# Optimization experiments

Hardware: AMD Instinct MI355X
Metric: run time of the kernel (lower is better)

Reference implementation:

```python
import jax, jax.numpy as jnp
import numpy as np

R = 50000          # residues
P = 24             # residue_pad_length
APR = 15           # atoms per residue (<= P)
N = R * APR        # total atoms
ACD = ATD = RCD = RID = 32
N_ATOM_CODES, N_ATOM_TYPES, N_RES_CODES, MAX_SEQ = 38, 6, 21, 1024
VEC_OUT, SC_OUT = 64, 256          # irreps_out = 64x1e + 256x0e
SC_IN = P * ACD + P * ATD + RCD + RID  # 1600 scalar inputs


def setup_inputs() -> dict:
    key = jax.random.key(0)
    ks = jax.random.split(key, 10)
    return {
        "residue_base_coords": jax.random.normal(ks[0], (R, 3), jnp.float32),
        "residue_relative_coords": jax.random.normal(ks[1], (N, 3), jnp.float32),
        "residue_code_index": jax.random.randint(ks[2], (R,), 0, N_RES_CODES),
        "residue_sequence_index": jnp.arange(R) % MAX_SEQ,
        "atom_code_index": jax.random.randint(ks[3], (N,), 0, N_ATOM_CODES),
        "atom_type_index": jax.random.randint(ks[4], (N,), 0, N_ATOM_TYPES),
        "residue_index_atomwise": jnp.repeat(jnp.arange(R), APR),  # sorted, APR atoms each
        "W_atom_code": jax.random.normal(ks[5], (N_ATOM_CODES, ACD), jnp.float32),
        "W_atom_type": jax.random.normal(ks[6], (N_ATOM_TYPES, ATD), jnp.float32),
        "W_res_code": jax.random.normal(ks[7], (N_RES_CODES, RCD), jnp.float32),
        "W_res_idx": jax.random.normal(ks[8], (MAX_SEQ, RID), jnp.float32),
        "W_vec": jax.random.normal(jax.random.fold_in(key, 1), (P, VEC_OUT), jnp.float32),
        "W_sc": jax.random.normal(ks[9], (SC_IN, SC_OUT), jnp.float32),
    }


def reference(residue_base_coords, residue_relative_coords, residue_code_index,
              residue_sequence_index, atom_code_index, atom_type_index,
              residue_index_atomwise, W_atom_code, W_atom_type, W_res_code,
              W_res_idx, W_vec, W_sc):
    R_ = residue_base_coords.shape[0]
    P_ = W_vec.shape[0]
    N_ = residue_index_atomwise.shape[0]
    ri = residue_index_atomwise
    # vectorized replacement of the per-residue python loop:
    # position of each atom within its residue (residue_index_atomwise is sorted)
    offsets = jnp.searchsorted(ri, jnp.arange(R_))            # first atom of each residue
    pos = jnp.arange(N_) - offsets[ri]                        # [N]
    # scatter atoms into padded [R, P, ...] layout (pad slots stay 0, like F.pad)
    mask = jnp.zeros((R_, P_), bool).at[ri, pos].set(True)
    rel = jnp.zeros((R_, P_, 3), residue_relative_coords.dtype).at[ri, pos].set(residue_relative_coords)
    codes = jnp.zeros((R_, P_), atom_code_index.dtype).at[ri, pos].set(atom_code_index)
    types = jnp.zeros((R_, P_), atom_type_index.dtype).at[ri, pos].set(atom_type_index)
    maskf = mask.astype(W_atom_code.dtype)[..., None]
    # embedding lookups, masked (pad embeddings zeroed as in the torch code)
    ac = (W_atom_code[codes] * maskf).reshape(R_, -1)         # [R, P*ACD]
    at = (W_atom_type[types] * maskf).reshape(R_, -1)         # [R, P*ATD]
    rc = W_res_code[residue_code_index]                       # [R, RCD]
    rix = W_res_idx[residue_sequence_index]                   # [R, RID]
    scalars = jnp.concatenate([ac, at, rc, rix], axis=-1)     # [R, SC_IN]
    # e3nn o3.Linear: l=1 channels mix only with l=1 (Px1e -> VEC_OUTx1e),
    # l=0 channels mix only with l=0; path-normalized by sqrt(fan_in), no bias.
    out_vec = jnp.einsum('rpc,pm->rmc', rel, W_vec) / jnp.sqrt(jnp.float32(P_))
    out_sc = (scalars @ W_sc) / jnp.sqrt(jnp.float32(scalars.shape[-1]))
    features = jnp.concatenate([out_vec.reshape(R_, -1), out_sc], axis=-1)  # [R, 3*VEC_OUT+SC_OUT]
    return residue_base_coords, features  # ResidueState(coords, features)
```

## Files before the change

kernel.cpp:

```cpp
#include <hip/hip_runtime.h>
#include <stdint.h>

static constexpr int P       = 24;
static constexpr int EMB_D   = 32;
static constexpr int N_AC    = 38;
static constexpr int N_AT    = 6;
static constexpr int N_RC    = 21;
static constexpr int MAXSEQ  = 1024;
static constexpr int VEC_OUT = 64;
static constexpr int SC_OUT  = 256;
static constexpr int FEAT    = 3 * VEC_OUT + SC_OUT;
static constexpr int CT      = N_AC * N_AT;
static constexpr int NROWS   = P * CT;
static constexpr int ROWB    = SC_OUT * 2;
static constexpr uint32_t ZROWB = (uint32_t)NROWS * ROWB;
static constexpr uint32_t EOFS  = (uint32_t)N_RC * 512;

__device__ __forceinline__ unsigned short f2bf(float f) {
    uint32_t x = __float_as_uint(f);
    uint32_t r = (x + 0x7FFFu + ((x >> 16) & 1u)) >> 16;
    return (unsigned short)r;
}

__global__ __launch_bounds__(256) void k1_init_build(
        const float* __restrict__ Wac, const float* __restrict__ Wat,
        const float* __restrict__ Wrc, const float* __restrict__ Wri,
        const float* __restrict__ Wsc,
        float* __restrict__ Ec, float* __restrict__ Et,
        unsigned short* __restrict__ ErcH, unsigned short* __restrict__ ErixH,
        int* __restrict__ starts, int* __restrict__ ends, int R) {
    int b = blockIdx.x;
    const int initB = (R + 255) / 256;
    if (b < initB) {
        int i = b * 256 + threadIdx.x;
        if (i < R) { starts[i] = 0; ends[i] = 0; }
        return;
    }
    b -= initB;
    const float* Wemb; int n_emb, sc_base, idx, sect;
    if (b < P * N_AC) {
        Wemb = Wac; n_emb = N_AC; sc_base = 0; idx = b; sect = 0;
    } else if (b < P * N_AC + P * N_AT) {
        Wemb = Wat; n_emb = N_AT; sc_base = P * EMB_D; idx = b - P * N_AC; sect = 1;
    } else if (b < P * N_AC + P * N_AT + N_RC) {
        Wemb = Wrc; n_emb = N_RC; sc_base = 2 * P * EMB_D;
        idx = b - (P * N_AC + P * N_AT); sect = 2;
    } else {
        Wemb = Wri; n_emb = MAXSEQ; sc_base = 2 * P * EMB_D + EMB_D;
        idx = b - (P * N_AC + P * N_AT + N_RC); sect = 3;
    }
    int p = idx / n_emb, e = idx % n_emb;
    int o = threadIdx.x;
    const float* wrow = Wemb + (size_t)e * EMB_D;
    const float* scol = Wsc + (size_t)(sc_base + p * EMB_D) * SC_OUT + o;
    float s = 0.f;
#pragma unroll
    for (int d = 0; d < EMB_D; ++d) s += wrow[d] * scol[(size_t)d * SC_OUT];
    s *= 0.025f;
    if (sect == 0)      Ec[(size_t)idx * SC_OUT + o] = s;
    else if (sect == 1) Et[(size_t)idx * SC_OUT + o] = s;
    else if (sect == 2) ErcH[(size_t)idx * SC_OUT + o] = f2bf(s);
    else                ErixH[(size_t)idx * SC_OUT + o] = f2bf(s);
}

__global__ void k2_find_bounds(const int* __restrict__ ri, int* __restrict__ starts,
                               int* __restrict__ ends, int N) {
    int i = blockIdx.x * blockDim.x + threadIdx.x;
    if (i >= N) return;
    int r = ri[i];
    if (i == 0 || ri[i - 1] != r) starts[r] = i;
    if (i == N - 1 || ri[i + 1] != r) ends[r] = i + 1;
}

__global__ __launch_bounds__(256) void k3_fuse_prep(
        const float* __restrict__ Ec, const float* __restrict__ Et,
        unsigned short* __restrict__ Etab,
        const int* __restrict__ starts, const int* __restrict__ ends,
        const int* __restrict__ rcode, const int* __restrict__ rseq,
        const int* __restrict__ acode, const int* __restrict__ atype,
        const float* __restrict__ rel, const float* __restrict__ base,
        float* __restrict__ out_coords,
        int4* __restrict__ hdr, uint32_t* __restrict__ recArr, int R) {
    int b = blockIdx.x;
    if (b < NROWS + 1) {
        int o = threadIdx.x;
        if (b == NROWS) { Etab[(size_t)b * SC_OUT + o] = 0; return; }
        int j = b / CT, ct = b % CT, c = ct / N_AT, t = ct % N_AT;
        float s = Ec[((size_t)j * N_AC + c) * SC_OUT + o] +
                  Et[((size_t)j * N_AT + t) * SC_OUT + o];
        Etab[(size_t)b * SC_OUT + o] = f2bf(s);
        return;
    }
    b -= NROWS + 1;
    const int hdrB = (R + 255) >> 8;
    if (b < hdrB) {
        int i = b * 256 + threadIdx.x;
        if (i < R) {
            int st = starts[i];
            int c = ends[i] - st; if (c > P) c = P;
            hdr[i] = make_int4(st, c, rcode[i], rseq[i]);
        }
        return;
    }
    b -= hdrB;
    const int coordB = (3 * R + 1023) >> 10;
    if (b < coordB) {
        int i = b * 256 + threadIdx.x;
        int n4 = (3 * R) >> 2;
        if (i < n4)
            reinterpret_cast<float4*>(out_coords)[i] =
                reinterpret_cast<const float4*>(base)[i];
        if (i == n4) {
            for (int t = 4 * n4; t < 3 * R; ++t) out_coords[t] = base[t];
        }
        return;
    }
    b -= coordB;
    int i = b * 256 + threadIdx.x;
    if (i >= R * 64) return;
    int r = i >> 6, l = i & 63;
    int st = starts[r];
    int c = ends[r] - st; if (c > P) c = P;
    uint32_t out;
    if (l < 16) {
        out = ZROWB;
        if (l < c)
            out = (uint32_t)((l * CT + acode[st + l] * N_AT + atype[st + l]) * ROWB);
    } else {
        int idx = l - 16, k = idx / 3, cc = idx - k * 3;
        float v = 0.f;
        if (k < c) v = rel[(size_t)(st + k) * 3 + cc];
        out = __float_as_uint(v);
    }
    recArr[(size_t)r * 64 + l] = out;
}

struct F3 { float x, y, z; };

#define RELV(RV, I) (((I) & 3) == 0 ? RV[(I) >> 2].x : \
                     ((I) & 3) == 1 ? RV[(I) >> 2].y : \
                     ((I) & 3) == 2 ? RV[(I) >> 2].z : RV[(I) >> 2].w)

__global__ __launch_bounds__(256, 4) void k4_residue(
        const int4* __restrict__ hdr, const uint32_t* __restrict__ recArr,
        const unsigned char* __restrict__ tab,
        const unsigned char* __restrict__ ErcBase,
        const float* __restrict__ Wvec,
        const int* __restrict__ acode, const int* __restrict__ atype,
        const float* __restrict__ rel,
        float* __restrict__ out_feat, int R) {

    __shared__ float lds_w[16 * VEC_OUT];
    for (int t = threadIdx.x; t < 16 * VEC_OUT; t += 256) lds_w[t] = Wvec[t];
    __syncthreads();

    const int wave   = (blockIdx.x << 2) + (threadIdx.x >> 6);
    const int lane   = threadIdx.x & 63;
    const int b31    = lane & 31;
    const bool hiH   = lane >= 32;
    const uint32_t lo16 = (uint32_t)(b31 * 16);
    const int totalw = gridDim.x << 2;
    if (wave >= R) return;

    int j  = wave;
    int rr = __builtin_amdgcn_readfirstlane(j < R ? j : R - 1);
    uint32_t rec = recArr[(size_t)rr * 64 + (lane & 15)];
    int4 h = hdr[rr];

    while (true) {
        const float4* srel = reinterpret_cast<const float4*>(
            recArr + (size_t)rr * 64 + 16);
        float4 rv[12];
#pragma unroll
        for (int q = 0; q < 12; ++q) rv[q] = srel[q];

        uint4 g0, g1, g2, g3, g4, g5, g6, g7, g8;
#define PG(GK, K)                                                              \
        {                                                                      \
            uint32_t re = (uint32_t)__builtin_amdgcn_readlane((int)rec, 2*(K));   \
            uint32_t ro = (uint32_t)__builtin_amdgcn_readlane((int)rec, 2*(K)+1); \
            GK = *reinterpret_cast<const uint4*>(tab + (hiH ? ro : re) + lo16);   \
        }
        PG(g0, 0) PG(g1, 1) PG(g2, 2) PG(g3, 3)
        PG(g4, 4) PG(g5, 5) PG(g6, 6) PG(g7, 7)
#undef PG
        {
            uint32_t vo = (hiH ? EOFS + ((uint32_t)h.w << 9)
                               : ((uint32_t)h.z << 9)) + lo16;
            g8 = *reinterpret_cast<const uint4*>(ErcBase + vo);
        }

        int jn = j + totalw;
        int r1 = __builtin_amdgcn_readfirstlane(jn < R ? jn : R - 1);
        uint32_t recN = recArr[(size_t)r1 * 64 + (lane & 15)];
        int4 hN = hdr[r1];

        float vx = 0.f, vy = 0.f, vz = 0.f;
#pragma unroll
        for (int k = 0; k < 16; ++k) {
            float wk = lds_w[k * VEC_OUT + lane];
            vx = fmaf(RELV(rv, 3 * k), wk, vx);
            vy = fmaf(RELV(rv, 3 * k + 1), wk, vy);
            vz = fmaf(RELV(rv, 3 * k + 2), wk, vz);
        }

        float a0 = 0.f, a1 = 0.f, a2 = 0.f, a3 = 0.f;
        float a4 = 0.f, a5 = 0.f, a6 = 0.f, a7 = 0.f;
#define PACC(GK)                                                               \
        a0 += __uint_as_float(GK.x << 16);                                     \
        a1 += __uint_as_float(GK.x & 0xFFFF0000u);                             \
        a2 += __uint_as_float(GK.y << 16);                                     \
        a3 += __uint_as_float(GK.y & 0xFFFF0000u);                             \
        a4 += __uint_as_float(GK.z << 16);                                     \
        a5 += __uint_as_float(GK.z & 0xFFFF0000u);                             \
        a6 += __uint_as_float(GK.w << 16);                                     \
        a7 += __uint_as_float(GK.w & 0xFFFF0000u);
        PACC(g0) PACC(g1) PACC(g2) PACC(g3) PACC(g4)
        PACC(g5) PACC(g6) PACC(g7) PACC(g8)
#undef PACC

        a0 += __shfl_xor(a0, 32); a1 += __shfl_xor(a1, 32);
        a2 += __shfl_xor(a2, 32); a3 += __shfl_xor(a3, 32);
        a4 += __shfl_xor(a4, 32); a5 += __shfl_xor(a5, 32);
        a6 += __shfl_xor(a6, 32); a7 += __shfl_xor(a7, 32);

        if (h.y > 16) {
            int st = h.x;
            for (int k = 16; k < h.y; ++k) {
                int c = acode[st + k], t = atype[st + k];
                const unsigned char* rp = tab +
                    (uint32_t)((k * CT + c * N_AT + t) * ROWB) + lo16;
                uint4 gg = *reinterpret_cast<const uint4*>(rp);
                float wk = Wvec[k * VEC_OUT + lane];
                vx = fmaf(rel[(size_t)(st + k) * 3], wk, vx);
                vy = fmaf(rel[(size_t)(st + k) * 3 + 1], wk, vy);
                vz = fmaf(rel[(size_t)(st + k) * 3 + 2], wk, vz);
                a0 += __uint_as_float(gg.x << 16);
                a1 += __uint_as_float(gg.x & 0xFFFF0000u);
                a2 += __uint_as_float(gg.y << 16);
                a3 += __uint_as_float(gg.y & 0xFFFF0000u);
                a4 += __uint_as_float(gg.z << 16);
                a5 += __uint_as_float(gg.z & 0xFFFF0000u);
                a6 += __uint_as_float(gg.w << 16);
                a7 += __uint_as_float(gg.w & 0xFFFF0000u);
            }
        }

        const float vs = 0.20412414523193150818f;
        float* frow = out_feat + (size_t)j * FEAT;
        F3 v3; v3.x = vx * vs; v3.y = vy * vs; v3.z = vz * vs;
        *reinterpret_cast<F3*>(frow + 3 * lane) = v3;
        float4 sd = hiH ? make_float4(a4, a5, a6, a7)
                        : make_float4(a0, a1, a2, a3);
        uint32_t so = ((uint32_t)b31 << 5) + (hiH ? 16u : 0u);
        *reinterpret_cast<float4*>(
            reinterpret_cast<char*>(frow + 3 * VEC_OUT) + so) = sd;

        j = jn;
        if (j >= R) break;
        rec = recN; h = hN; rr = r1;
    }
}

extern "C" void kernel_launch(void* const* d_in, const int* in_sizes, int n_in,
                              void* d_out, int out_size, void* d_ws, size_t ws_size,
                              hipStream_t stream) {
    const float* base  = (const float*)d_in[0];
    const float* rel   = (const float*)d_in[1];
    const int*   rcode = (const int*)d_in[2];
    const int*   rseq  = (const int*)d_in[3];
    const int*   acode = (const int*)d_in[4];
    const int*   atype = (const int*)d_in[5];
    const int*   ri    = (const int*)d_in[6];
    const float* Wac   = (const float*)d_in[7];
    const float* Wat   = (const float*)d_in[8];
    const float* Wrc   = (const float*)d_in[9];
    const float* Wri   = (const float*)d_in[10];
    const float* Wv    = (const float*)d_in[11];
    const float* Wsc   = (const float*)d_in[12];

    const int R = in_sizes[0] / 3;
    const int N = in_sizes[6];

    float* out_coords = (float*)d_out;
    float* out_feat   = out_coords + (size_t)R * 3;

    char* ws = (char*)d_ws;
    size_t ofs = 0;
    auto alloc = [&](size_t bytes) {
        void* p = ws + ofs;
        ofs = (ofs + bytes + 255) & ~255ULL;
        return p;
    };
    int*            starts = (int*)alloc((size_t)R * 4);
    int*            ends   = (int*)alloc((size_t)R * 4);
    float*          Ec_f   = (float*)alloc((size_t)P * N_AC * SC_OUT * 4);
    float*          Et_f   = (float*)alloc((size_t)P * N_AT * SC_OUT * 4);
    unsigned short* ErcH   = (unsigned short*)alloc((size_t)N_RC * SC_OUT * 2);
    unsigned short* ErixH  = (unsigned short*)alloc((size_t)MAXSEQ * SC_OUT * 2);
    unsigned short* Etab   = (unsigned short*)alloc((size_t)(NROWS + 1) * SC_OUT * 2);
    int4*           hdr    = (int4*)alloc((size_t)R * 16);
    uint32_t*       recArr = (uint32_t*)alloc((size_t)R * 64 * 4);
    (void)ws_size; (void)n_in; (void)out_size;

    const int initB  = (R + 255) / 256;
    const int k1B    = initB + P * N_AC + P * N_AT + N_RC + MAXSEQ;
    const int hdrB   = (R + 255) / 256;
    const int coordB = (3 * R + 1023) / 1024;
    const int recB   = (R * 64 + 255) / 256;
    const int k3B    = (NROWS + 1) + hdrB + coordB + recB;

    k1_init_build<<<k1B, 256, 0, stream>>>(Wac, Wat, Wrc, Wri, Wsc,
                                           Ec_f, Et_f, ErcH, ErixH, starts, ends, R);
    k2_find_bounds<<<(N + 255) / 256, 256, 0, stream>>>(ri, starts, ends, N);
    k3_fuse_prep<<<k3B, 256, 0, stream>>>(Ec_f, Et_f, Etab, starts, ends,
                                          rcode, rseq, acode, atype, rel, base,
                                          out_coords, hdr, recArr, R);
    k4_residue<<<2048, 256, 0, stream>>>(
        hdr, recArr, (const unsigned char*)Etab,
        (const unsigned char*)ErcH, Wv, acode, atype, rel, out_feat, R);
}
```

Measured before the change: 65.29 us.

## Build fused bf16 atom table directly in k1 and read coords via readlane

The combined code+type projection table is now computed directly in the first kernel, instead of staging fp32 per-code and per-type tables and adding them in the prep kernel. This drops two intermediate buffers and their global round trip, at the cost of more FMA work per table row (5472 rows times 64 FMAs). In the main residue kernel each lane now loads one record word (full 64 lanes) and gets the relative coordinates by cross-lane readlane. This replaces a per-lane 12-float4 vector load and the register pressure that came with it.

```diff
diff --git a/kernel.cpp b/kernel.cpp
--- a/kernel.cpp
+++ b/kernel.cpp
@@ -22,45 +22,56 @@
     return (unsigned short)r;
 }
 
-__global__ __launch_bounds__(256) void k1_init_build(
+__global__ __launch_bounds__(256) void k1_build(
         const float* __restrict__ Wac, const float* __restrict__ Wat,
         const float* __restrict__ Wrc, const float* __restrict__ Wri,
         const float* __restrict__ Wsc,
-        float* __restrict__ Ec, float* __restrict__ Et,
+        unsigned short* __restrict__ Etab,
         unsigned short* __restrict__ ErcH, unsigned short* __restrict__ ErixH,
         int* __restrict__ starts, int* __restrict__ ends, int R) {
     int b = blockIdx.x;
     const int initB = (R + 255) / 256;
+    const int o = threadIdx.x;
     if (b < initB) {
-        int i = b * 256 + threadIdx.x;
+        int i = b * 256 + o;
         if (i < R) { starts[i] = 0; ends[i] = 0; }
         return;
     }
     b -= initB;
-    const float* Wemb; int n_emb, sc_base, idx, sect;
-    if (b < P * N_AC) {
-        Wemb = Wac; n_emb = N_AC; sc_base = 0; idx = b; sect = 0;
-    } else if (b < P * N_AC + P * N_AT) {
-        Wemb = Wat; n_emb = N_AT; sc_base = P * EMB_D; idx = b - P * N_AC; sect = 1;
-    } else if (b < P * N_AC + P * N_AT + N_RC) {
-        Wemb = Wrc; n_emb = N_RC; sc_base = 2 * P * EMB_D;
-        idx = b - (P * N_AC + P * N_AT); sect = 2;
-    } else {
-        Wemb = Wri; n_emb = MAXSEQ; sc_base = 2 * P * EMB_D + EMB_D;
-        idx = b - (P * N_AC + P * N_AT + N_RC); sect = 3;
-    }
-    int p = idx / n_emb, e = idx % n_emb;
-    int o = threadIdx.x;
-    const float* wrow = Wemb + (size_t)e * EMB_D;
-    const float* scol = Wsc + (size_t)(sc_base + p * EMB_D) * SC_OUT + o;
-    float s = 0.f;
-#pragma unroll
-    for (int d = 0; d < EMB_D; ++d) s += wrow[d] * scol[(size_t)d * SC_OUT];
-    s *= 0.025f;
-    if (sect == 0)      Ec[(size_t)idx * SC_OUT + o] = s;
-    else if (sect == 1) Et[(size_t)idx * SC_OUT + o] = s;
-    else if (sect == 2) ErcH[(size_t)idx * SC_OUT + o] = f2bf(s);
-    else                ErixH[(size_t)idx * SC_OUT + o] = f2bf(s);
+    if (b < NROWS + 1) {
+        if (b == NROWS) { Etab[(size_t)b * SC_OUT + o] = 0; return; }
+        int j = b / CT, ct = b % CT, c = ct / N_AT, t = ct % N_AT;
+        const float* wc = Wac + (size_t)c * EMB_D;
+        const float* wt = Wat + (size_t)t * EMB_D;
+        const float* sc_c = Wsc + (size_t)(j * EMB_D) * SC_OUT + o;
+        const float* sc_t = Wsc + (size_t)(P * EMB_D + j * EMB_D) * SC_OUT + o;
+        float s = 0.f;
+#pragma unroll
+        for (int d = 0; d < EMB_D; ++d) s += wc[d] * sc_c[(size_t)d * SC_OUT];
+#pragma unroll
+        for (int d = 0; d < EMB_D; ++d) s += wt[d] * sc_t[(size_t)d * SC_OUT];
+        Etab[(size_t)b * SC_OUT + o] = f2bf(s * 0.025f);
+        return;
+    }
+    b -= NROWS + 1;
+    if (b < N_RC) {
+        const float* wr = Wrc + (size_t)b * EMB_D;
+        const float* sc = Wsc + (size_t)(2 * P * EMB_D) * SC_OUT + o;
+        float s = 0.f;
+#pragma unroll
+        for (int d = 0; d < EMB_D; ++d) s += wr[d] * sc[(size_t)d * SC_OUT];
+        ErcH[(size_t)b * SC_OUT + o] = f2bf(s * 0.025f);
+        return;
+    }
+    b -= N_RC;
+    {
+        const float* wr = Wri + (size_t)b * EMB_D;
+        const float* sc = Wsc + (size_t)(2 * P * EMB_D + EMB_D) * SC_OUT + o;
+        float s = 0.f;
+#pragma unroll
+        for (int d = 0; d < EMB_D; ++d) s += wr[d] * sc[(size_t)d * SC_OUT];
+        ErixH[(size_t)b * SC_OUT + o] = f2bf(s * 0.025f);
+    }
 }
 
 __global__ void k2_find_bounds(const int* __restrict__ ri, int* __restrict__ starts,
@@ -72,9 +83,7 @@
     if (i == N - 1 || ri[i + 1] != r) ends[r] = i + 1;
 }
 
-__global__ __launch_bounds__(256) void k3_fuse_prep(
-        const float* __restrict__ Ec, const float* __restrict__ Et,
-        unsigned short* __restrict__ Etab,
+__global__ __launch_bounds__(256) void k3_prep(
         const int* __restrict__ starts, const int* __restrict__ ends,
         const int* __restrict__ rcode, const int* __restrict__ rseq,
         const int* __restrict__ acode, const int* __restrict__ atype,
@@ -82,16 +91,6 @@
         float* __restrict__ out_coords,
         int4* __restrict__ hdr, uint32_t* __restrict__ recArr, int R) {
     int b = blockIdx.x;
-    if (b < NROWS + 1) {
-        int o = threadIdx.x;
-        if (b == NROWS) { Etab[(size_t)b * SC_OUT + o] = 0; return; }
-        int j = b / CT, ct = b % CT, c = ct / N_AT, t = ct % N_AT;
-        float s = Ec[((size_t)j * N_AC + c) * SC_OUT + o] +
-                  Et[((size_t)j * N_AT + t) * SC_OUT + o];
-        Etab[(size_t)b * SC_OUT + o] = f2bf(s);
-        return;
-    }
-    b -= NROWS + 1;
     const int hdrB = (R + 255) >> 8;
     if (b < hdrB) {
         int i = b * 256 + threadIdx.x;
@@ -137,10 +136,6 @@
 
 struct F3 { float x, y, z; };
 
-#define RELV(RV, I) (((I) & 3) == 0 ? RV[(I) >> 2].x : \
-                     ((I) & 3) == 1 ? RV[(I) >> 2].y : \
-                     ((I) & 3) == 2 ? RV[(I) >> 2].z : RV[(I) >> 2].w)
-
 __global__ __launch_bounds__(256, 4) void k4_residue(
         const int4* __restrict__ hdr, const uint32_t* __restrict__ recArr,
         const unsigned char* __restrict__ tab,
@@ -162,18 +157,18 @@
     const int totalw = gridDim.x << 2;
     if (wave >= R) return;
 
-    int j  = wave;
-    int rr = __builtin_amdgcn_readfirstlane(j < R ? j : R - 1);
-    uint32_t rec = recArr[(size_t)rr * 64 + (lane & 15)];
-    int4 h = hdr[rr];
-
+    uint32_t rec, recN;
+    int4 h, hN;
+
+    auto REC = [&](uint32_t& rc, int4& hh, int j) {
+        int rr = __builtin_amdgcn_readfirstlane(j < R ? j : R - 1);
+        hh = hdr[rr];
+        rc = recArr[(size_t)rr * 64 + lane];
+    };
+
+    int j = wave;
+    REC(rec, h, j);
     while (true) {
-        const float4* srel = reinterpret_cast<const float4*>(
-            recArr + (size_t)rr * 64 + 16);
-        float4 rv[12];
-#pragma unroll
-        for (int q = 0; q < 12; ++q) rv[q] = srel[q];
-
         uint4 g0, g1, g2, g3, g4, g5, g6, g7, g8;
 #define PG(GK, K)                                                              \
         {                                                                      \
@@ -191,17 +186,18 @@
         }
 
         int jn = j + totalw;
-        int r1 = __builtin_amdgcn_readfirstlane(jn < R ? jn : R - 1);
-        uint32_t recN = recArr[(size_t)r1 * 64 + (lane & 15)];
-        int4 hN = hdr[r1];
+        REC(recN, hN, jn);
 
         float vx = 0.f, vy = 0.f, vz = 0.f;
 #pragma unroll
         for (int k = 0; k < 16; ++k) {
+            float sx = __uint_as_float((uint32_t)__builtin_amdgcn_readlane((int)rec, 16 + 3 * k));
+            float sy = __uint_as_float((uint32_t)__builtin_amdgcn_readlane((int)rec, 17 + 3 * k));
+            float sz = __uint_as_float((uint32_t)__builtin_amdgcn_readlane((int)rec, 18 + 3 * k));
             float wk = lds_w[k * VEC_OUT + lane];
-            vx = fmaf(RELV(rv, 3 * k), wk, vx);
-            vy = fmaf(RELV(rv, 3 * k + 1), wk, vy);
-            vz = fmaf(RELV(rv, 3 * k + 2), wk, vz);
+            vx = fmaf(sx, wk, vx);
+            vy = fmaf(sy, wk, vy);
+            vz = fmaf(sz, wk, vz);
         }
 
         float a0 = 0.f, a1 = 0.f, a2 = 0.f, a3 = 0.f;
@@ -258,7 +254,7 @@
 
         j = jn;
         if (j >= R) break;
-        rec = recN; h = hN; rr = r1;
+        rec = recN; h = hN;
     }
 }
 
@@ -294,8 +290,6 @@
     };
     int*            starts = (int*)alloc((size_t)R * 4);
     int*            ends   = (int*)alloc((size_t)R * 4);
-    float*          Ec_f   = (float*)alloc((size_t)P * N_AC * SC_OUT * 4);
-    float*          Et_f   = (float*)alloc((size_t)P * N_AT * SC_OUT * 4);
     unsigned short* ErcH   = (unsigned short*)alloc((size_t)N_RC * SC_OUT * 2);
     unsigned short* ErixH  = (unsigned short*)alloc((size_t)MAXSEQ * SC_OUT * 2);
     unsigned short* Etab   = (unsigned short*)alloc((size_t)(NROWS + 1) * SC_OUT * 2);
@@ -304,18 +298,17 @@
     (void)ws_size; (void)n_in; (void)out_size;
 
     const int initB  = (R + 255) / 256;
-    const int k1B    = initB + P * N_AC + P * N_AT + N_RC + MAXSEQ;
+    const int k1B    = initB + (NROWS + 1) + N_RC + MAXSEQ;
     const int hdrB   = (R + 255) / 256;
     const int coordB = (3 * R + 1023) / 1024;
     const int recB   = (R * 64 + 255) / 256;
-    const int k3B    = (NROWS + 1) + hdrB + coordB + recB;
-
-    k1_init_build<<<k1B, 256, 0, stream>>>(Wac, Wat, Wrc, Wri, Wsc,
-                                           Ec_f, Et_f, ErcH, ErixH, starts, ends, R);
+    const int k3B    = hdrB + coordB + recB;
+
+    k1_build<<<k1B, 256, 0, stream>>>(Wac, Wat, Wrc, Wri, Wsc,
+                                      Etab, ErcH, ErixH, starts, ends, R);
     k2_find_bounds<<<(N + 255) / 256, 256, 0, stream>>>(ri, starts, ends, N);
-    k3_fuse_prep<<<k3B, 256, 0, stream>>>(Ec_f, Et_f, Etab, starts, ends,
-                                          rcode, rseq, acode, atype, rel, base,
-                                          out_coords, hdr, recArr, R);
+    k3_prep<<<k3B, 256, 0, stream>>>(starts, ends, rcode, rseq, acode, atype,
+                                     rel, base, out_coords, hdr, recArr, R);
     k4_residue<<<2048, 256, 0, stream>>>(
         hdr, recArr, (const unsigned char*)Etab,
         (const unsigned char*)ErcH, Wv, acode, atype, rel, out_feat, R);
```

Measured after the change: 71.99 us. 1.1x slower.
